# Kernel tuning notes

Hardware: AMD Instinct MI355X
Metric: run time of the kernel (lower is better)

The kernel has to match this reference:

```python
import jax, jax.numpy as jnp
import numpy as np

N_NODES = 100_000
N_EDGES = 800_000
NODE_DIM = 192
CONF_DIM = 64
HID = 256  # graphsage_in == graphsage_hidden
ALPHA = 0.2  # LeakyReLU negative slope


def _lrelu(x):
    return jnp.where(x >= 0, x, ALPHA * x)


def _sage_max(x, src, dst, wl, bl, wr):
    # PyG SAGEConv, aggr='max': out = lin_l(max_{j in N(i)} x_j) + lin_r(x_i)
    msgs = x[src]                                   # [E, HID] gather
    agg = jax.ops.segment_max(msgs, dst, num_segments=N_NODES)  # [N, HID]
    agg = jnp.where(jnp.isneginf(agg), 0.0, agg)    # isolated nodes -> 0
    return agg @ wl + bl + x @ wr


def _mlp2(x, w0, b0, w1, b1):
    # Linear -> LeakyReLU(0.2) -> Linear (activation only between layers)
    return _lrelu(x @ w0 + b0) @ w1 + b1


def setup_inputs() -> dict:
    key = jax.random.key(0)
    ks = jax.random.split(key, 16)
    s = 0.05
    inp = {
        "node_features": jax.random.normal(ks[0], (N_NODES, NODE_DIM), jnp.float32),
        "config_features": jax.random.normal(ks[1], (N_NODES, CONF_DIM), jnp.float32),
        "edges": jax.random.randint(ks[2], (2, N_EDGES), 0, N_NODES, jnp.int32),
        "prenet_w0": jax.random.normal(ks[3], (HID, NODE_DIM), jnp.float32) * s,
        "prenet_b0": jnp.zeros((NODE_DIM,), jnp.float32),
        "prenet_w1": jax.random.normal(ks[4], (NODE_DIM, NODE_DIM), jnp.float32) * s,
        "prenet_b1": jnp.zeros((NODE_DIM,), jnp.float32),
    }
    for l, k0 in ((0, 5), (1, 10)):
        inp[f"sage{l}_wl"] = jax.random.normal(ks[k0], (HID, HID), jnp.float32) * s
        inp[f"sage{l}_bl"] = jnp.zeros((HID,), jnp.float32)
        inp[f"sage{l}_wr"] = jax.random.normal(ks[k0 + 1], (HID, HID), jnp.float32) * s
        inp[f"mlp{l}_w0"] = jax.random.normal(ks[k0 + 2], (HID, NODE_DIM), jnp.float32) * s
        inp[f"mlp{l}_b0"] = jnp.zeros((NODE_DIM,), jnp.float32)
        inp[f"mlp{l}_w1"] = jax.random.normal(ks[k0 + 3], (NODE_DIM, NODE_DIM), jnp.float32) * s
        inp[f"mlp{l}_b1"] = jnp.zeros((NODE_DIM,), jnp.float32)
    return inp


def reference(node_features, config_features, edges,
              prenet_w0, prenet_b0, prenet_w1, prenet_b1,
              sage0_wl, sage0_bl, sage0_wr, mlp0_w0, mlp0_b0, mlp0_w1, mlp0_b1,
              sage1_wl, sage1_bl, sage1_wr, mlp1_w0, mlp1_b0, mlp1_w1, mlp1_b1):
    src, dst = edges[0], edges[1]
    x = jnp.concatenate([config_features, node_features], axis=1)  # [N, 256]
    x = _lrelu(_mlp2(x, prenet_w0, prenet_b0, prenet_w1, prenet_b1))  # [N, 192]
    layers = [
        (sage0_wl, sage0_bl, sage0_wr, mlp0_w0, mlp0_b0, mlp0_w1, mlp0_b1),
        (sage1_wl, sage1_bl, sage1_wr, mlp1_w0, mlp1_b0, mlp1_w1, mlp1_b1),
    ]
    for swl, sbl, swr, mw0, mb0, mw1, mb1 in layers:
        y = jnp.concatenate([config_features, x], axis=1)          # [N, 256]
        y = _sage_max(y, src, dst, swl, sbl, swr)                  # [N, 256]
        y = _lrelu(_mlp2(y, mw0, mb0, mw1, mb1))                   # [N, 192]
        x = x + y
    return x
```

## Files before the change

kernel.cpp:

```cpp
#include <hip/hip_runtime.h>
#include <stdint.h>

#define N_NODES 100000
#define N_EDGES 800000

typedef unsigned short u16;
typedef __attribute__((ext_vector_type(8))) short bf16x8;
typedef __attribute__((ext_vector_type(8))) unsigned short ushort8;
typedef __attribute__((ext_vector_type(4))) float f32x4;
typedef __attribute__((ext_vector_type(4))) int i32x4;
typedef __attribute__((ext_vector_type(4))) unsigned int u32x4;

struct alignas(8) U16x4 { u16 x, y, z, w; };

__device__ __forceinline__ u16 f2b(float f) {
    union { float f; unsigned u; } x; x.f = f;
    unsigned r = (x.u + 0x7FFFu + ((x.u >> 16) & 1u)) >> 16;
    return (u16)r;
}
__device__ __forceinline__ float b2f(u16 h) {
    union { unsigned u; float f; } x; x.u = ((unsigned)h) << 16;
    return x.f;
}
__device__ __forceinline__ u16 keyb(u16 h) {
    u16 m = (u16)((short)h >> 15);
    return (u16)(h ^ (0x8000u | (m & 0x7FFFu)));
}
__device__ __forceinline__ u16 unkey(u16 k) {
    u16 m = (u16)((short)k >> 15);
    return (u16)(k ^ (0x8000u | (~m & 0x7FFFu)));
}
__device__ __forceinline__ unsigned pkmax(unsigned a, unsigned b) {
    unsigned d;
    asm("v_pk_max_u16 %0, %1, %2" : "=v"(d) : "v"(a), "v"(b));
    return d;
}
__device__ __forceinline__ u32x4 pkmax4(u32x4 a, u32x4 b) {
    u32x4 r;
    r.x = pkmax(a.x, b.x); r.y = pkmax(a.y, b.y);
    r.z = pkmax(a.z, b.z); r.w = pkmax(a.w, b.w);
    return r;
}

__device__ __forceinline__ void gload_lds16(const void* g, void* l) {
    __builtin_amdgcn_global_load_lds(
        (const __attribute__((address_space(1))) char*)(uintptr_t)g,
        (__attribute__((address_space(3))) char*)(uintptr_t)l,
        16, 0, 0);
}

__device__ __forceinline__ int simgG(int row, int col) { return row * 136 + col; }
__device__ __forceinline__ int simgF(int row, int col) { return row * 200 + col; }


__global__ void k_prep(const float* __restrict__ conf, const float* __restrict__ node,
                       u16* __restrict__ conf16, u16* __restrict__ node16,
                       u16* __restrict__ keyed, int* __restrict__ deg) {
    const int c4 = N_NODES * 64 / 4;
    const int n4 = N_NODES * 192 / 4;
    int i = blockIdx.x * blockDim.x + threadIdx.x;
    if (i < c4) {
        float4 v = ((const float4*)conf)[i];
        U16x4 o; o.x = f2b(v.x); o.y = f2b(v.y); o.z = f2b(v.z); o.w = f2b(v.w);
        ((U16x4*)conf16)[i] = o;
        U16x4 ko; ko.x = keyb(o.x); ko.y = keyb(o.y); ko.z = keyb(o.z); ko.w = keyb(o.w);
        int n = i >> 4;
        ((U16x4*)keyed)[n * 64 + (i & 15)] = ko;
    } else if (i < c4 + n4) {
        float4 v = ((const float4*)node)[i - c4];
        U16x4 o; o.x = f2b(v.x); o.y = f2b(v.y); o.z = f2b(v.z); o.w = f2b(v.w);
        ((U16x4*)node16)[i - c4] = o;
    } else if (i < c4 + n4 + N_NODES / 4) {
        i32x4 z = {0, 0, 0, 0};
        ((i32x4*)deg)[i - c4 - n4] = z;
    }
}


struct PackSeg { const float* a; const float* b; u16* dst; int K0, K1, Ncol, beg, end; };
struct PackArgs { PackSeg s[8]; };

__global__ void k_pack(PackArgs p, int total) {
    int idx = blockIdx.x * blockDim.x + threadIdx.x;
    if (idx >= total) return;
    #pragma unroll
    for (int si = 0; si < 8; ++si) {
        if (idx >= p.s[si].beg && idx < p.s[si].end) {
            int li = idx - p.s[si].beg;
            int Ncol = p.s[si].Ncol, K0 = p.s[si].K0;
            int kq = li & 7;
            int t = li >> 3;
            int c15 = t & 15; t >>= 4;
            int k8 = t & 3;  t >>= 2;
            int nb = Ncol >> 4;
            int cb = t % nb;
            int ks = t / nb;
            int col = cb * 16 + c15;
            int k = ks * 32 + k8 * 8 + kq;
            float v = (k < K0) ? p.s[si].a[(size_t)k * Ncol + col]
                               : p.s[si].b[(size_t)(k - K0) * Ncol + col];
            p.s[si].dst[li] = f2b(v);
        }
    }
}


__global__ void k_count(const int* __restrict__ dst, int* __restrict__ deg) {
    int e = blockIdx.x * blockDim.x + threadIdx.x;
    if (e < N_EDGES) atomicAdd(&deg[dst[e]], 1);
}

__global__ void k_scan1(const int* __restrict__ deg, int* __restrict__ excl,
                        int* __restrict__ bsum, int n) {
    __shared__ int sh[512];
    int t = threadIdx.x;
    int base = blockIdx.x * 2048 + t * 4;
    int v0 = (base + 0 < n) ? deg[base + 0] : 0;
    int v1 = (base + 1 < n) ? deg[base + 1] : 0;
    int v2 = (base + 2 < n) ? deg[base + 2] : 0;
    int v3 = (base + 3 < n) ? deg[base + 3] : 0;
    int tot = v0 + v1 + v2 + v3;
    sh[t] = tot;
    __syncthreads();
    for (int off = 1; off < 512; off <<= 1) {
        int x = (t >= off) ? sh[t - off] : 0;
        __syncthreads();
        sh[t] += x;
        __syncthreads();
    }
    int run = sh[t] - tot;
    if (base + 0 < n) excl[base + 0] = run; run += v0;
    if (base + 1 < n) excl[base + 1] = run; run += v1;
    if (base + 2 < n) excl[base + 2] = run; run += v2;
    if (base + 3 < n) excl[base + 3] = run;
    if (t == 511) bsum[blockIdx.x] = sh[t];
}

__global__ void k_scan2(int* __restrict__ bsum, int nb) {
    __shared__ int sh[64];
    int t = threadIdx.x;
    int v = (t < nb) ? bsum[t] : 0;
    sh[t] = v;
    __syncthreads();
    for (int off = 1; off < 64; off <<= 1) {
        int x = (t >= off) ? sh[t - off] : 0;
        __syncthreads();
        sh[t] += x;
        __syncthreads();
    }
    if (t < nb) bsum[t] = sh[t] - v;
}

__global__ void k_scan3(int* __restrict__ excl, const int* __restrict__ bsum,
                        int* __restrict__ cursor, int n) {
    int i = blockIdx.x * blockDim.x + threadIdx.x;
    if (i < n) {
        int v = excl[i] + bsum[i >> 11];
        excl[i] = v;
        cursor[i] = v;
    }
}

__global__ void k_scatter(const int* __restrict__ src, const int* __restrict__ dst,
                          int* __restrict__ cursor, int* __restrict__ esrc) {
    int e = blockIdx.x * blockDim.x + threadIdx.x;
    if (e < N_EDGES) {
        int p = atomicAdd(&cursor[dst[e]], 1);
        esrc[p] = src[e];
    }
}


template<int CHUNKS>
__global__ __launch_bounds__(256) void k_agg(
    const u16* __restrict__ keyed,
    const int* __restrict__ indptr, const int* __restrict__ deg,
    const int* __restrict__ iend, const int* __restrict__ esrc,
    u16* __restrict__ agg, u16* __restrict__ aggC) {
    __shared__ int se[512];
    __shared__ int sinfo[2];
    const int b4 = blockIdx.x * 4;
    if (threadIdx.x == 0) {
        sinfo[0] = indptr[b4];
        sinfo[1] = iend[b4 + 3];
    }
    __syncthreads();
    const int sbase = sinfo[0];
    const int slen = sinfo[1] - sbase;
    const bool useLds = slen <= 512;
    if (useLds) {
        for (int i = threadIdx.x; i < slen; i += 256) se[i] = esrc[sbase + i];
    }
    __syncthreads();

    const int node = b4 + (threadIdx.x >> 6);
    const int lane = threadIdx.x & 63;
    constexpr int ACTIVE = (CHUNKS == 32) ? 64 : 48;
    const int e_sub = (CHUNKS == 32) ? (lane >> 5) : (lane >= 24 ? 1 : 0);
    int ch = lane - e_sub * CHUNKS;
    if (ch < 0 || ch >= CHUNKS) ch = 0;
    const int start = indptr[node];
    const int d = deg[node];
    const u16* bp = keyed + ((CHUNKS == 32) ? 0 : 64) + ch * 8;

    u32x4 m = {0u, 0u, 0u, 0u};

    if (lane < ACTIVE && d > 0) {
        const int rounds = (d + 7) >> 3;
        const int lbase = start - sbase;
        for (int rr = 0; rr < rounds; ++rr) {
            const int b0 = rr * 8 + e_sub;
            const int dm1 = d - 1;
            int i0 = min(b0, dm1), i1 = min(b0 + 2, dm1);
            int i2 = min(b0 + 4, dm1), i3 = min(b0 + 6, dm1);
            int s0, s1, s2, s3;
            if (useLds) {
                s0 = se[lbase + i0]; s1 = se[lbase + i1];
                s2 = se[lbase + i2]; s3 = se[lbase + i3];
            } else {
                s0 = esrc[start + i0]; s1 = esrc[start + i1];
                s2 = esrc[start + i2]; s3 = esrc[start + i3];
            }
            u32x4 v0 = *(const u32x4*)(bp + (size_t)s0 * 256);
            u32x4 v1 = *(const u32x4*)(bp + (size_t)s1 * 256);
            u32x4 v2 = *(const u32x4*)(bp + (size_t)s2 * 256);
            u32x4 v3 = *(const u32x4*)(bp + (size_t)s3 * 256);
            m = pkmax4(m, pkmax4(pkmax4(v0, v1), pkmax4(v2, v3)));
        }
    }

    if (CHUNKS == 32) {
        m.x = pkmax(m.x, __shfl_xor(m.x, 32, 64));
        m.y = pkmax(m.y, __shfl_xor(m.y, 32, 64));
        m.z = pkmax(m.z, __shfl_xor(m.z, 32, 64));
        m.w = pkmax(m.w, __shfl_xor(m.w, 32, 64));
    } else {
        m.x = pkmax(m.x, __shfl(m.x, lane + 24, 64));
        m.y = pkmax(m.y, __shfl(m.y, lane + 24, 64));
        m.z = pkmax(m.z, __shfl(m.z, lane + 24, 64));
        m.w = pkmax(m.w, __shfl(m.w, lane + 24, 64));
    }

    unsigned wv[4] = {m.x, m.y, m.z, m.w};
    ushort8 o;
    #pragma unroll
    for (int j = 0; j < 4; ++j) {
        u16 klo = (u16)(wv[j] & 0xFFFFu), khi = (u16)(wv[j] >> 16);
        o[2 * j]     = (d > 0) ? unkey(klo) : (u16)0;
        o[2 * j + 1] = (d > 0) ? unkey(khi) : (u16)0;
    }

    if (CHUNKS == 32) {
        if (lane < 32) {
            *(ushort8*)(agg + (size_t)node * 256 + lane * 8) = o;
            if (lane < 8)
                *(ushort8*)(aggC + (size_t)node * 64 + lane * 8) = o;
        }
    } else {
        if (lane < 24) {
            *(ushort8*)(agg + (size_t)node * 256 + 64 + lane * 8) = o;
        } else if (lane >= 48 && lane < 56) {
            const int c2 = lane - 48;
            ushort8 v = *(const ushort8*)(aggC + (size_t)node * 64 + c2 * 8);
            *(ushort8*)(agg + (size_t)node * 256 + c2 * 8) = v;
        }
    }
}


template<int BN>
__global__ __launch_bounds__(512) void k_gemm(
    const u16* __restrict__ A0, int K0,
    const u16* __restrict__ A1, int K1,
    const u16* __restrict__ A2, int K2,
    const u16* __restrict__ Bt,
    const float* __restrict__ bias,
    u16* __restrict__ outb,
    int nrows)
{
    constexpr int FN = BN / 64;
    constexpr int ASZ = 128 * 32;
    __shared__ u16 lds[2][ASZ + BN * 32] __attribute__((aligned(16)));

    const int tid = threadIdx.x;
    const int wave = tid >> 6;
    const int lane = tid & 63;
    const int wr = wave >> 2;
    const int wc = wave & 3;
    const int rowbase = blockIdx.x * 128;
    const int nk = (K0 + K1 + K2) >> 5;

    const int arow = ((tid >> 6) << 4) | (tid & 15);
    int grow = rowbase + arow; if (grow >= nrows) grow = nrows - 1;
    const int ak8 = (tid >> 4) & 3;
    const u16* segp[3] = {A0, A1, A2};
    const int segK[3] = {K0, K1, K2};
    int seg = 0;
    const u16* gA = segp[0] + (size_t)grow * segK[0] + ak8 * 8;
    int segleft = segK[0] >> 5;
    const u16* gB0 = Bt + (size_t)tid * 8;
    const u16* gB1 = Bt + (size_t)(512 + tid) * 8;
    const int wb = wave * 512;

    auto adv = [&]() {
        gA += 32;
        if (--segleft == 0) {
            while (seg < 2) {
                ++seg;
                if (segK[seg] > 0) {
                    gA = segp[seg] + (size_t)grow * segK[seg] + ak8 * 8;
                    segleft = segK[seg] >> 5;
                    break;
                }
            }
        }
        gB0 += BN * 32;
        gB1 += BN * 32;
    };
    auto stage = [&](int buf) {
        gload_lds16(gA, &lds[buf][wb]);
        gload_lds16(gB0, &lds[buf][ASZ + wb]);
        if constexpr (BN == 256) {
            gload_lds16(gB1, &lds[buf][ASZ + 4096 + wb]);
        } else {
            if (tid < 256) gload_lds16(gB1, &lds[buf][ASZ + 4096 + wb]);
        }
    };

    f32x4 zero = {0.f, 0.f, 0.f, 0.f};
    f32x4 acc[4][FN];
    #pragma unroll
    for (int fm = 0; fm < 4; ++fm)
        #pragma unroll
        for (int fn = 0; fn < FN; ++fn)
            acc[fm][fn] = zero;

    stage(0); adv();
    __syncthreads();

    const int l15 = lane & 15, l4 = lane >> 4;

    for (int ks = 0; ks < nk; ++ks) {
        const int cur = ks & 1;
        if (ks + 1 < nk) { stage(cur ^ 1); adv(); }
        const u16* la = &lds[cur][0];
        const u16* lb = &lds[cur][ASZ];
        bf16x8 a[4], b[FN];
        #pragma unroll
        for (int fm = 0; fm < 4; ++fm)
            a[fm] = *(const bf16x8*)(la + (wr * 4 + fm) * 512 + lane * 8);
        #pragma unroll
        for (int fn = 0; fn < FN; ++fn)
            b[fn] = *(const bf16x8*)(lb + (wc * FN + fn) * 512 + lane * 8);
        #pragma unroll
        for (int fm = 0; fm < 4; ++fm)
            #pragma unroll
            for (int fn = 0; fn < FN; ++fn)
                acc[fm][fn] = __builtin_amdgcn_mfma_f32_16x16x32_bf16(a[fm], b[fn], acc[fm][fn], 0, 0, 0);
        __syncthreads();
    }

    u16* sbuf = &lds[0][0];
    #pragma unroll
    for (int chunk = 0; chunk < 2; ++chunk) {
        if ((wc >> 1) == chunk) {
            const int cbase = (wc & 1) * 64;
            #pragma unroll
            for (int fn = 0; fn < FN; ++fn) {
                const int cp = cbase + fn * 16 + l15;
                const float bs = bias[chunk * 128 + cp];
                #pragma unroll
                for (int fm = 0; fm < 4; ++fm) {
                    const int rbase = wr * 64 + fm * 16 + l4 * 4;
                    #pragma unroll
                    for (int r = 0; r < 4; ++r)
                        sbuf[simgG(rbase + r, cp)] = f2b(acc[fm][fn][r] + bs);
                }
            }
        }
        __syncthreads();
        #pragma unroll
        for (int j = 0; j < 4; ++j) {
            const int chk = j * 512 + tid;
            const int row = chk >> 4;
            const int cp = (chk & 15) * 8;
            const int gr = rowbase + row;
            if (gr < nrows) {
                ushort8 hv = *(const ushort8*)&sbuf[simgG(row, cp)];
                *(ushort8*)(outb + (size_t)gr * 256 + chunk * 128 + cp) = hv;
            }
        }
        __syncthreads();
    }
}


template<int EPI>
__global__ __launch_bounds__(512) void k_fused(
    const u16* __restrict__ A0, int K0,
    const u16* __restrict__ A1, int K1,
    const u16* __restrict__ B1t, const float* __restrict__ bias1,
    const u16* __restrict__ B2t, const float* __restrict__ bias2,
    float* __restrict__ outf, u16* __restrict__ outb,
    const u16* __restrict__ resid16, u16* __restrict__ keyed,
    int nrows)
{
    __shared__ u16 lds[25592] __attribute__((aligned(16)));

    const int tid = threadIdx.x;
    const int wave = tid >> 6;
    const int lane = tid & 63;
    const int wr = wave >> 2;
    const int wc = wave & 3;
    const int l15 = lane & 15, l4 = lane >> 4;
    const int rowbase = blockIdx.x * 128;
    const int nk1 = (K0 + K1) >> 5;

    const int arow = ((tid >> 6) << 4) | (tid & 15);
    int grow = rowbase + arow; if (grow >= nrows) grow = nrows - 1;
    const int ak8 = (tid >> 4) & 3;
    const u16* gA = A0 + (size_t)grow * K0 + ak8 * 8;
    int segleft = K0 >> 5;
    const u16* gB0 = B1t + (size_t)tid * 8;
    const u16* gB1 = B1t + (size_t)(512 + tid) * 8;
    const int wb = wave * 512;

    auto adv = [&]() {
        gA += 32;
        if (--segleft == 0 && K1 > 0) {
            gA = A1 + (size_t)grow * K1 + ak8 * 8;
            segleft = K1 >> 5;
        }
        gB0 += 6144;
        gB1 += 6144;
    };
    auto stage = [&](int buf) {
        gload_lds16(gA, &lds[buf * 4096 + wb]);
        gload_lds16(gB0, &lds[8192 + buf * 6144 + wb]);
        if (tid < 256) gload_lds16(gB1, &lds[8192 + buf * 6144 + 4096 + wb]);
    };

    f32x4 zero = {0.f, 0.f, 0.f, 0.f};
    f32x4 acc[4][3];
    #pragma unroll
    for (int fm = 0; fm < 4; ++fm)
        #pragma unroll
        for (int fn = 0; fn < 3; ++fn)
            acc[fm][fn] = zero;

    stage(0); adv();
    __syncthreads();

    for (int ks = 0; ks < nk1; ++ks) {
        const int cur = ks & 1;
        if (ks + 1 < nk1) { stage(cur ^ 1); adv(); }
        const u16* la = &lds[cur * 4096];
        const u16* lb = &lds[8192 + cur * 6144];
        bf16x8 a[4], b[3];
        #pragma unroll
        for (int fm = 0; fm < 4; ++fm)
            a[fm] = *(const bf16x8*)(la + (wr * 4 + fm) * 512 + lane * 8);
        #pragma unroll
        for (int fn = 0; fn < 3; ++fn)
            b[fn] = *(const bf16x8*)(lb + (wc * 3 + fn) * 512 + lane * 8);
        #pragma unroll
        for (int fm = 0; fm < 4; ++fm)
            #pragma unroll
            for (int fn = 0; fn < 3; ++fn)
                acc[fm][fn] = __builtin_amdgcn_mfma_f32_16x16x32_bf16(a[fm], b[fn], acc[fm][fn], 0, 0, 0);
        __syncthreads();
    }

    {
        const int c0 = wc * 48;
        #pragma unroll
        for (int fn = 0; fn < 3; ++fn) {
            const int c = c0 + fn * 16 + l15;
            const float bs = bias1[c];
            const int coff = (c >> 5) * 4096 + ((c >> 3) & 3) * 128 + (c & 7);
            #pragma unroll
            for (int fm = 0; fm < 4; ++fm) {
                const int rb = wr * 4 + fm;
                #pragma unroll
                for (int rr = 0; rr < 4; ++rr) {
                    const int r16 = l4 * 4 + rr;
                    float v = acc[fm][fn][rr] + bs;
                    v = (v >= 0.f) ? v : 0.2f * v;
                    lds[coff + rb * 512 + r16 * 8] = f2b(v);
                }
            }
        }
    }
    __syncthreads();

    bf16x8 breg[18];
    #pragma unroll
    for (int ks = 0; ks < 6; ++ks)
        #pragma unroll
        for (int fn = 0; fn < 3; ++fn)
            breg[ks * 3 + fn] = *(const bf16x8*)(B2t + (size_t)(ks * 12 + wc * 3 + fn) * 512 + lane * 8);

    f32x4 acc2[4][3];
    #pragma unroll
    for (int fm = 0; fm < 4; ++fm)
        #pragma unroll
        for (int fn = 0; fn < 3; ++fn)
            acc2[fm][fn] = zero;

    #pragma unroll
    for (int ks = 0; ks < 6; ++ks) {
        bf16x8 a2[4];
        #pragma unroll
        for (int fm = 0; fm < 4; ++fm)
            a2[fm] = *(const bf16x8*)(&lds[ks * 4096 + (wr * 4 + fm) * 512 + lane * 8]);
        #pragma unroll
        for (int fm = 0; fm < 4; ++fm)
            #pragma unroll
            for (int fn = 0; fn < 3; ++fn)
                acc2[fm][fn] = __builtin_amdgcn_mfma_f32_16x16x32_bf16(a2[fm], breg[ks * 3 + fn], acc2[fm][fn], 0, 0, 0);
    }
    __syncthreads();

    {
        const int c0 = wc * 48;
        #pragma unroll
        for (int fn = 0; fn < 3; ++fn) {
            const int c = c0 + fn * 16 + l15;
            const float bs = bias2[c];
            #pragma unroll
            for (int fm = 0; fm < 4; ++fm) {
                const int rbase = wr * 64 + fm * 16 + l4 * 4;
                #pragma unroll
                for (int r = 0; r < 4; ++r) {
                    float v = acc2[fm][fn][r] + bs;
                    v = (v >= 0.f) ? v : 0.2f * v;
                    lds[simgF(rbase + r, c)] = f2b(v);
                }
            }
        }
    }
    __syncthreads();

    #pragma unroll
    for (int j = 0; j < 6; ++j) {
        const int chk = j * 512 + tid;
        const int row = chk / 24;
        const int c = (chk - row * 24) * 8;
        const int gr = rowbase + row;
        if (gr < nrows) {
            ushort8 hv = *(const ushort8*)&lds[simgF(row, c)];
            if (EPI == 4) {
                ushort8 rv = *(const ushort8*)(resid16 + (size_t)gr * 192 + c);
                f32x4 o0, o1;
                #pragma unroll
                for (int k = 0; k < 4; ++k) {
                    o0[k] = b2f(hv[k]) + b2f(rv[k]);
                    o1[k] = b2f(hv[k + 4]) + b2f(rv[k + 4]);
                }
                *(f32x4*)(outf + (size_t)gr * 192 + c) = o0;
                *(f32x4*)(outf + (size_t)gr * 192 + c + 4) = o1;
            } else if (EPI == 5) {
                *(ushort8*)(outb + (size_t)gr * 192 + c) = hv;
                ushort8 kv;
                #pragma unroll
                for (int k = 0; k < 8; ++k) kv[k] = keyb(hv[k]);
                *(ushort8*)(keyed + (size_t)gr * 256 + 64 + c) = kv;
            } else {
                ushort8 rv = *(const ushort8*)(resid16 + (size_t)gr * 192 + c);
                ushort8 nb, kv;
                #pragma unroll
                for (int k = 0; k < 8; ++k) {
                    u16 hb = f2b(b2f(hv[k]) + b2f(rv[k]));
                    nb[k] = hb;
                    kv[k] = keyb(hb);
                }
                *(ushort8*)(outb + (size_t)gr * 192 + c) = nb;
                *(ushort8*)(keyed + (size_t)gr * 256 + 64 + c) = kv;
            }
        }
    }
}


extern "C" void kernel_launch(void* const* d_in, const int* in_sizes, int n_in,
                              void* d_out, int out_size, void* d_ws, size_t ws_size,
                              hipStream_t stream)
{
    (void)in_sizes; (void)n_in; (void)out_size; (void)ws_size;
    const float* node = (const float*)d_in[0];
    const float* conf = (const float*)d_in[1];
    const int* edges  = (const int*)d_in[2];
    const float* pw0  = (const float*)d_in[3];
    const float* pb0  = (const float*)d_in[4];
    const float* pw1  = (const float*)d_in[5];
    const float* pb1  = (const float*)d_in[6];
    const float* W[14];
    for (int i = 0; i < 14; ++i) W[i] = (const float*)d_in[7 + i];
    float* out = (float*)d_out;
    const int* e_src = edges;
    const int* e_dst = edges + N_EDGES;

    u16* keyed = (u16*)d_out;

    char* w = (char*)d_ws;
    auto alloc = [&](size_t b) { char* p = w; w += (b + 255) & ~(size_t)255; return p; };
    u16* conf16 = (u16*)alloc((size_t)N_NODES * 64 * 2);
    u16* node16 = (u16*)alloc((size_t)N_NODES * 192 * 2);
    u16* x16    = (u16*)alloc((size_t)N_NODES * 192 * 2);
    u16* agg16  = (u16*)alloc((size_t)N_NODES * 256 * 2);
    u16* aggC   = (u16*)alloc((size_t)N_NODES * 64 * 2);
    int* deg    = (int*)alloc((size_t)N_NODES * 4);
    int* indptr = (int*)alloc((size_t)N_NODES * 4);
    int* cursor = (int*)alloc((size_t)N_NODES * 4);
    int* esrc   = (int*)alloc((size_t)N_EDGES * 4);
    int* bsum   = (int*)alloc(4096);
    u16* pw0t   = (u16*)alloc((size_t)192 * 256 * 2);
    u16* pw1t   = (u16*)alloc((size_t)192 * 192 * 2);
    u16 *sB[2], *mw0t[2], *mw1t[2];
    for (int l = 0; l < 2; ++l) {
        sB[l]   = (u16*)alloc((size_t)256 * 512 * 2);
        mw0t[l] = (u16*)alloc((size_t)192 * 256 * 2);
        mw1t[l] = (u16*)alloc((size_t)192 * 192 * 2);
    }

    {
        const int tot = N_NODES * 64 / 4 + N_NODES * 192 / 4 + N_NODES / 4;
        k_prep<<<(tot + 255) / 256, 256, 0, stream>>>(conf, node, conf16, node16, keyed, deg);
    }
    {
        PackArgs pa;
        int off = 0;
        auto seg = [&](int i, const float* a, int K0, const float* b, int K1, int Ncol, u16* dst) {
            int sz = Ncol * (K0 + K1);
            pa.s[i] = {a, b, dst, K0, K1, Ncol, off, off + sz};
            off += sz;
        };
        seg(0, pw0, 256, nullptr, 0, 192, pw0t);
        seg(1, pw1, 192, nullptr, 0, 192, pw1t);
        seg(2, W[0], 256, W[2], 256, 256, sB[0]);
        seg(3, W[3], 256, nullptr, 0, 192, mw0t[0]);
        seg(4, W[5], 192, nullptr, 0, 192, mw1t[0]);
        seg(5, W[7], 256, W[9], 256, 256, sB[1]);
        seg(6, W[10], 256, nullptr, 0, 192, mw0t[1]);
        seg(7, W[12], 192, nullptr, 0, 192, mw1t[1]);
        k_pack<<<(off + 255) / 256, 256, 0, stream>>>(pa, off);
    }
    k_count<<<(N_EDGES + 255) / 256, 256, 0, stream>>>(e_dst, deg);
    int nb = (N_NODES + 2047) / 2048;
    k_scan1<<<nb, 512, 0, stream>>>(deg, indptr, bsum, N_NODES);
    k_scan2<<<1, 64, 0, stream>>>(bsum, nb);
    k_scan3<<<(N_NODES + 255) / 256, 256, 0, stream>>>(indptr, bsum, cursor, N_NODES);
    k_scatter<<<(N_EDGES + 255) / 256, 256, 0, stream>>>(e_src, e_dst, cursor, esrc);

    const int gblk = (N_NODES + 127) / 128;
    k_fused<5><<<gblk, 512, 0, stream>>>(conf16, 64, node16, 192,
                                         pw0t, pb0, pw1t, pb1,
                                         nullptr, x16, nullptr, keyed, N_NODES);
    for (int l = 0; l < 2; ++l) {
        if (l == 0)
            k_agg<32><<<N_NODES / 4, 256, 0, stream>>>(keyed, indptr, deg, cursor, esrc, agg16, aggC);
        else
            k_agg<24><<<N_NODES / 4, 256, 0, stream>>>(keyed, indptr, deg, cursor, esrc, agg16, aggC);
        k_gemm<256><<<gblk, 512, 0, stream>>>(agg16, 256, conf16, 64, x16, 192,
                                              sB[l], W[7*l+1], agg16, N_NODES);
        if (l == 0)
            k_fused<6><<<gblk, 512, 0, stream>>>(agg16, 256, nullptr, 0,
                                                 mw0t[0], W[4], mw1t[0], W[6],
                                                 nullptr, x16, x16, keyed, N_NODES);
        else
            k_fused<4><<<gblk, 512, 0, stream>>>(agg16, 256, nullptr, 0,
                                                 mw0t[1], W[11], mw1t[1], W[13],
                                                 out, nullptr, x16, nullptr, N_NODES);
    }
}
```

Before: 444.1 us.

## Fuse SAGE linear GEMM with following MLP into one per-layer kernel

Replaces the separate SAGE GEMM kernel and MLP kernel with a single k_layer kernel per layer. The SAGE output tile stays in LDS as bf16 and feeds the two MLP GEMMs directly, so the [N,256] intermediate is never written to or re-read from global memory. B weights are now loaded straight from global memory into registers with double buffering, not staged through LDS. This removes one launch and one round trip through global memory per layer, but it puts more pressure on registers and LDS (a single 80KB LDS buffer), which may reduce occupancy.

```diff
diff --git a/kernel.cpp b/kernel.cpp
--- a/kernel.cpp
+++ b/kernel.cpp
@@ -49,8 +49,10 @@
         16, 0, 0);
 }
 
-__device__ __forceinline__ int simgG(int row, int col) { return row * 136 + col; }
 __device__ __forceinline__ int simgF(int row, int col) { return row * 200 + col; }
+__device__ __forceinline__ int fimg(int row, int c) {
+    return (c >> 5) * 4096 + ((c >> 3) & 3) * 128 + (c & 7) + (row >> 4) * 512 + (row & 15) * 8;
+}
 
 
 __global__ void k_prep(const float* __restrict__ conf, const float* __restrict__ node,
@@ -268,133 +270,6 @@
 }
 
 
-template<int BN>
-__global__ __launch_bounds__(512) void k_gemm(
-    const u16* __restrict__ A0, int K0,
-    const u16* __restrict__ A1, int K1,
-    const u16* __restrict__ A2, int K2,
-    const u16* __restrict__ Bt,
-    const float* __restrict__ bias,
-    u16* __restrict__ outb,
-    int nrows)
-{
-    constexpr int FN = BN / 64;
-    constexpr int ASZ = 128 * 32;
-    __shared__ u16 lds[2][ASZ + BN * 32] __attribute__((aligned(16)));
-
-    const int tid = threadIdx.x;
-    const int wave = tid >> 6;
-    const int lane = tid & 63;
-    const int wr = wave >> 2;
-    const int wc = wave & 3;
-    const int rowbase = blockIdx.x * 128;
-    const int nk = (K0 + K1 + K2) >> 5;
-
-    const int arow = ((tid >> 6) << 4) | (tid & 15);
-    int grow = rowbase + arow; if (grow >= nrows) grow = nrows - 1;
-    const int ak8 = (tid >> 4) & 3;
-    const u16* segp[3] = {A0, A1, A2};
-    const int segK[3] = {K0, K1, K2};
-    int seg = 0;
-    const u16* gA = segp[0] + (size_t)grow * segK[0] + ak8 * 8;
-    int segleft = segK[0] >> 5;
-    const u16* gB0 = Bt + (size_t)tid * 8;
-    const u16* gB1 = Bt + (size_t)(512 + tid) * 8;
-    const int wb = wave * 512;
-
-    auto adv = [&]() {
-        gA += 32;
-        if (--segleft == 0) {
-            while (seg < 2) {
-                ++seg;
-                if (segK[seg] > 0) {
-                    gA = segp[seg] + (size_t)grow * segK[seg] + ak8 * 8;
-                    segleft = segK[seg] >> 5;
-                    break;
-                }
-            }
-        }
-        gB0 += BN * 32;
-        gB1 += BN * 32;
-    };
-    auto stage = [&](int buf) {
-        gload_lds16(gA, &lds[buf][wb]);
-        gload_lds16(gB0, &lds[buf][ASZ + wb]);
-        if constexpr (BN == 256) {
-            gload_lds16(gB1, &lds[buf][ASZ + 4096 + wb]);
-        } else {
-            if (tid < 256) gload_lds16(gB1, &lds[buf][ASZ + 4096 + wb]);
-        }
-    };
-
-    f32x4 zero = {0.f, 0.f, 0.f, 0.f};
-    f32x4 acc[4][FN];
-    #pragma unroll
-    for (int fm = 0; fm < 4; ++fm)
-        #pragma unroll
-        for (int fn = 0; fn < FN; ++fn)
-            acc[fm][fn] = zero;
-
-    stage(0); adv();
-    __syncthreads();
-
-    const int l15 = lane & 15, l4 = lane >> 4;
-
-    for (int ks = 0; ks < nk; ++ks) {
-        const int cur = ks & 1;
-        if (ks + 1 < nk) { stage(cur ^ 1); adv(); }
-        const u16* la = &lds[cur][0];
-        const u16* lb = &lds[cur][ASZ];
-        bf16x8 a[4], b[FN];
-        #pragma unroll
-        for (int fm = 0; fm < 4; ++fm)
-            a[fm] = *(const bf16x8*)(la + (wr * 4 + fm) * 512 + lane * 8);
-        #pragma unroll
-        for (int fn = 0; fn < FN; ++fn)
-            b[fn] = *(const bf16x8*)(lb + (wc * FN + fn) * 512 + lane * 8);
-        #pragma unroll
-        for (int fm = 0; fm < 4; ++fm)
-            #pragma unroll
-            for (int fn = 0; fn < FN; ++fn)
-                acc[fm][fn] = __builtin_amdgcn_mfma_f32_16x16x32_bf16(a[fm], b[fn], acc[fm][fn], 0, 0, 0);
-        __syncthreads();
-    }
-
-    u16* sbuf = &lds[0][0];
-    #pragma unroll
-    for (int chunk = 0; chunk < 2; ++chunk) {
-        if ((wc >> 1) == chunk) {
-            const int cbase = (wc & 1) * 64;
-            #pragma unroll
-            for (int fn = 0; fn < FN; ++fn) {
-                const int cp = cbase + fn * 16 + l15;
-                const float bs = bias[chunk * 128 + cp];
-                #pragma unroll
-                for (int fm = 0; fm < 4; ++fm) {
-                    const int rbase = wr * 64 + fm * 16 + l4 * 4;
-                    #pragma unroll
-                    for (int r = 0; r < 4; ++r)
-                        sbuf[simgG(rbase + r, cp)] = f2b(acc[fm][fn][r] + bs);
-                }
-            }
-        }
-        __syncthreads();
-        #pragma unroll
-        for (int j = 0; j < 4; ++j) {
-            const int chk = j * 512 + tid;
-            const int row = chk >> 4;
-            const int cp = (chk & 15) * 8;
-            const int gr = rowbase + row;
-            if (gr < nrows) {
-                ushort8 hv = *(const ushort8*)&sbuf[simgG(row, cp)];
-                *(ushort8*)(outb + (size_t)gr * 256 + chunk * 128 + cp) = hv;
-            }
-        }
-        __syncthreads();
-    }
-}
-
-
 template<int EPI>
 __global__ __launch_bounds__(512) void k_fused(
     const u16* __restrict__ A0, int K0,
@@ -477,16 +352,14 @@
         for (int fn = 0; fn < 3; ++fn) {
             const int c = c0 + fn * 16 + l15;
             const float bs = bias1[c];
-            const int coff = (c >> 5) * 4096 + ((c >> 3) & 3) * 128 + (c & 7);
             #pragma unroll
             for (int fm = 0; fm < 4; ++fm) {
                 const int rb = wr * 4 + fm;
                 #pragma unroll
                 for (int rr = 0; rr < 4; ++rr) {
-                    const int r16 = l4 * 4 + rr;
                     float v = acc[fm][fn][rr] + bs;
                     v = (v >= 0.f) ? v : 0.2f * v;
-                    lds[coff + rb * 512 + r16 * 8] = f2b(v);
+                    lds[fimg(rb * 16 + l4 * 4 + rr, c)] = f2b(v);
                 }
             }
         }
@@ -549,8 +422,222 @@
         const int gr = rowbase + row;
         if (gr < nrows) {
             ushort8 hv = *(const ushort8*)&lds[simgF(row, c)];
+            *(ushort8*)(outb + (size_t)gr * 192 + c) = hv;
+            ushort8 kv;
+            #pragma unroll
+            for (int k = 0; k < 8; ++k) kv[k] = keyb(hv[k]);
+            *(ushort8*)(keyed + (size_t)gr * 256 + 64 + c) = kv;
+        }
+    }
+    (void)outf; (void)resid16;
+}
+
+
+template<int EPI>
+__global__ __launch_bounds__(512) void k_layer(
+    const u16* __restrict__ A0, const u16* __restrict__ A1, const u16* __restrict__ A2,
+    const u16* __restrict__ sBt, const float* __restrict__ bl,
+    const u16* __restrict__ B1t, const float* __restrict__ bias1,
+    const u16* __restrict__ B2t, const float* __restrict__ bias2,
+    float* __restrict__ outf, u16* __restrict__ outb,
+    const u16* __restrict__ resid16, u16* __restrict__ keyed,
+    int nrows)
+{
+    __shared__ u16 lds[40960] __attribute__((aligned(16)));
+
+    const int tid = threadIdx.x;
+    const int wave = tid >> 6;
+    const int lane = tid & 63;
+    const int wr = wave >> 2;
+    const int wc = wave & 3;
+    const int l15 = lane & 15, l4 = lane >> 4;
+    const int rowbase = blockIdx.x * 128;
+
+    const int arow = (wave << 4) | (tid & 15);
+    int grow = rowbase + arow; if (grow >= nrows) grow = nrows - 1;
+    const int ak8 = (tid >> 4) & 3;
+    const u16* segp[3] = {A0, A1, A2};
+    const int segK[3] = {256, 64, 192};
+    int seg = 0;
+    const u16* gA = segp[0] + (size_t)grow * 256 + ak8 * 8;
+    int segleft = 256 >> 5;
+    const int wb = wave * 512;
+    auto advA = [&]() {
+        gA += 32;
+        if (--segleft == 0 && seg < 2) {
+            ++seg;
+            gA = segp[seg] + (size_t)grow * segK[seg] + ak8 * 8;
+            segleft = segK[seg] >> 5;
+        }
+    };
+
+    f32x4 zero = {0.f, 0.f, 0.f, 0.f};
+    f32x4 acc[4][4];
+    #pragma unroll
+    for (int fm = 0; fm < 4; ++fm)
+        #pragma unroll
+        for (int fn = 0; fn < 4; ++fn)
+            acc[fm][fn] = zero;
+
+    gload_lds16(gA, &lds[wb]); advA();
+    bf16x8 bb[2][4];
+    #pragma unroll
+    for (int fn = 0; fn < 4; ++fn)
+        bb[0][fn] = *(const bf16x8*)(sBt + (size_t)(wc * 4 + fn) * 512 + lane * 8);
+    __syncthreads();
+
+    #pragma unroll
+    for (int ks = 0; ks < 16; ++ks) {
+        const int cur = ks & 1;
+        if (ks + 1 < 16) {
+            gload_lds16(gA, &lds[(cur ^ 1) * 4096 + wb]); advA();
+            #pragma unroll
+            for (int fn = 0; fn < 4; ++fn)
+                bb[cur ^ 1][fn] = *(const bf16x8*)(sBt + (size_t)((ks + 1) * 16 + wc * 4 + fn) * 512 + lane * 8);
+        }
+        bf16x8 a[4];
+        #pragma unroll
+        for (int fm = 0; fm < 4; ++fm)
+            a[fm] = *(const bf16x8*)(&lds[cur * 4096 + (wr * 4 + fm) * 512 + lane * 8]);
+        #pragma unroll
+        for (int fm = 0; fm < 4; ++fm)
+            #pragma unroll
+            for (int fn = 0; fn < 4; ++fn)
+                acc[fm][fn] = __builtin_amdgcn_mfma_f32_16x16x32_bf16(a[fm], bb[cur][fn], acc[fm][fn], 0, 0, 0);
+        __syncthreads();
+    }
+
+    {
+        const int c0 = wc * 64;
+        #pragma unroll
+        for (int fn = 0; fn < 4; ++fn) {
+            const int c = c0 + fn * 16 + l15;
+            const float bs = bl[c];
+            #pragma unroll
+            for (int fm = 0; fm < 4; ++fm) {
+                const int rb = wr * 4 + fm;
+                #pragma unroll
+                for (int rr = 0; rr < 4; ++rr)
+                    lds[8192 + fimg(rb * 16 + l4 * 4 + rr, c)] = f2b(acc[fm][fn][rr] + bs);
+            }
+        }
+    }
+    __syncthreads();
+
+    f32x4 acc2[4][3];
+    #pragma unroll
+    for (int fm = 0; fm < 4; ++fm)
+        #pragma unroll
+        for (int fn = 0; fn < 3; ++fn)
+            acc2[fm][fn] = zero;
+
+    bf16x8 b2[2][3];
+    #pragma unroll
+    for (int fn = 0; fn < 3; ++fn)
+        b2[0][fn] = *(const bf16x8*)(B1t + (size_t)(wc * 3 + fn) * 512 + lane * 8);
+
+    #pragma unroll
+    for (int ks = 0; ks < 8; ++ks) {
+        const int cur = ks & 1;
+        if (ks + 1 < 8) {
+            #pragma unroll
+            for (int fn = 0; fn < 3; ++fn)
+                b2[cur ^ 1][fn] = *(const bf16x8*)(B1t + (size_t)((ks + 1) * 12 + wc * 3 + fn) * 512 + lane * 8);
+        }
+        bf16x8 a2[4];
+        #pragma unroll
+        for (int fm = 0; fm < 4; ++fm)
+            a2[fm] = *(const bf16x8*)(&lds[8192 + ks * 4096 + (wr * 4 + fm) * 512 + lane * 8]);
+        #pragma unroll
+        for (int fm = 0; fm < 4; ++fm)
+            #pragma unroll
+            for (int fn = 0; fn < 3; ++fn)
+                acc2[fm][fn] = __builtin_amdgcn_mfma_f32_16x16x32_bf16(a2[fm], b2[cur][fn], acc2[fm][fn], 0, 0, 0);
+    }
+    __syncthreads();
+
+    {
+        const int c0 = wc * 48;
+        #pragma unroll
+        for (int fn = 0; fn < 3; ++fn) {
+            const int c = c0 + fn * 16 + l15;
+            const float bs = bias1[c];
+            #pragma unroll
+            for (int fm = 0; fm < 4; ++fm) {
+                const int rb = wr * 4 + fm;
+                #pragma unroll
+                for (int rr = 0; rr < 4; ++rr) {
+                    float v = acc2[fm][fn][rr] + bs;
+                    v = (v >= 0.f) ? v : 0.2f * v;
+                    lds[8192 + fimg(rb * 16 + l4 * 4 + rr, c)] = f2b(v);
+                }
+            }
+        }
+    }
+    __syncthreads();
+
+    f32x4 acc3[4][3];
+    #pragma unroll
+    for (int fm = 0; fm < 4; ++fm)
+        #pragma unroll
+        for (int fn = 0; fn < 3; ++fn)
+            acc3[fm][fn] = zero;
+
+    bf16x8 b3[2][3];
+    #pragma unroll
+    for (int fn = 0; fn < 3; ++fn)
+        b3[0][fn] = *(const bf16x8*)(B2t + (size_t)(wc * 3 + fn) * 512 + lane * 8);
+
+    #pragma unroll
+    for (int ks = 0; ks < 6; ++ks) {
+        const int cur = ks & 1;
+        if (ks + 1 < 6) {
+            #pragma unroll
+            for (int fn = 0; fn < 3; ++fn)
+                b3[cur ^ 1][fn] = *(const bf16x8*)(B2t + (size_t)((ks + 1) * 12 + wc * 3 + fn) * 512 + lane * 8);
+        }
+        bf16x8 a3[4];
+        #pragma unroll
+        for (int fm = 0; fm < 4; ++fm)
+            a3[fm] = *(const bf16x8*)(&lds[8192 + ks * 4096 + (wr * 4 + fm) * 512 + lane * 8]);
+        #pragma unroll
+        for (int fm = 0; fm < 4; ++fm)
+            #pragma unroll
+            for (int fn = 0; fn < 3; ++fn)
+                acc3[fm][fn] = __builtin_amdgcn_mfma_f32_16x16x32_bf16(a3[fm], b3[cur][fn], acc3[fm][fn], 0, 0, 0);
+    }
+    __syncthreads();
+
+    {
+        const int c0 = wc * 48;
+        #pragma unroll
+        for (int fn = 0; fn < 3; ++fn) {
+            const int c = c0 + fn * 16 + l15;
+            const float bs = bias2[c];
+            #pragma unroll
+            for (int fm = 0; fm < 4; ++fm) {
+                const int rbase = wr * 64 + fm * 16 + l4 * 4;
+                #pragma unroll
+                for (int r = 0; r < 4; ++r) {
+                    float v = acc3[fm][fn][r] + bs;
+                    v = (v >= 0.f) ? v : 0.2f * v;
+                    lds[8192 + simgF(rbase + r, c)] = f2b(v);
+                }
+            }
+        }
+    }
+    __syncthreads();
+
+    #pragma unroll
+    for (int j = 0; j < 6; ++j) {
+        const int chk = j * 512 + tid;
+        const int row = chk / 24;
+        const int c = (chk - row * 24) * 8;
+        const int gr = rowbase + row;
+        if (gr < nrows) {
+            ushort8 hv = *(const ushort8*)&lds[8192 + simgF(row, c)];
+            ushort8 rv = *(const ushort8*)(resid16 + (size_t)gr * 192 + c);
             if (EPI == 4) {
-                ushort8 rv = *(const ushort8*)(resid16 + (size_t)gr * 192 + c);
                 f32x4 o0, o1;
                 #pragma unroll
                 for (int k = 0; k < 4; ++k) {
@@ -559,14 +646,7 @@
                 }
                 *(f32x4*)(outf + (size_t)gr * 192 + c) = o0;
                 *(f32x4*)(outf + (size_t)gr * 192 + c + 4) = o1;
-            } else if (EPI == 5) {
-                *(ushort8*)(outb + (size_t)gr * 192 + c) = hv;
-                ushort8 kv;
-                #pragma unroll
-                for (int k = 0; k < 8; ++k) kv[k] = keyb(hv[k]);
-                *(ushort8*)(keyed + (size_t)gr * 256 + 64 + c) = kv;
             } else {
-                ushort8 rv = *(const ushort8*)(resid16 + (size_t)gr * 192 + c);
                 ushort8 nb, kv;
                 #pragma unroll
                 for (int k = 0; k < 8; ++k) {
@@ -656,20 +736,12 @@
     k_fused<5><<<gblk, 512, 0, stream>>>(conf16, 64, node16, 192,
                                          pw0t, pb0, pw1t, pb1,
                                          nullptr, x16, nullptr, keyed, N_NODES);
-    for (int l = 0; l < 2; ++l) {
-        if (l == 0)
-            k_agg<32><<<N_NODES / 4, 256, 0, stream>>>(keyed, indptr, deg, cursor, esrc, agg16, aggC);
-        else
-            k_agg<24><<<N_NODES / 4, 256, 0, stream>>>(keyed, indptr, deg, cursor, esrc, agg16, aggC);
-        k_gemm<256><<<gblk, 512, 0, stream>>>(agg16, 256, conf16, 64, x16, 192,
-                                              sB[l], W[7*l+1], agg16, N_NODES);
-        if (l == 0)
-            k_fused<6><<<gblk, 512, 0, stream>>>(agg16, 256, nullptr, 0,
-                                                 mw0t[0], W[4], mw1t[0], W[6],
-                                                 nullptr, x16, x16, keyed, N_NODES);
-        else
-            k_fused<4><<<gblk, 512, 0, stream>>>(agg16, 256, nullptr, 0,
-                                                 mw0t[1], W[11], mw1t[1], W[13],
-                                                 out, nullptr, x16, nullptr, N_NODES);
-    }
-}
+    k_agg<32><<<N_NODES / 4, 256, 0, stream>>>(keyed, indptr, deg, cursor, esrc, agg16, aggC);
+    k_layer<6><<<gblk, 512, 0, stream>>>(agg16, conf16, x16,
+                                         sB[0], W[1], mw0t[0], W[4], mw1t[0], W[6],
+                                         nullptr, x16, x16, keyed, N_NODES);
+    k_agg<24><<<N_NODES / 4, 256, 0, stream>>>(keyed, indptr, deg, cursor, esrc, agg16, aggC);
+    k_layer<4><<<gblk, 512, 0, stream>>>(agg16, conf16, x16,
+                                         sB[1], W[8], mw0t[1], W[11], mw1t[1], W[13],
+                                         out, nullptr, x16, nullptr, N_NODES);
+}
```

New measurement: 469.7 us. 5.8% more time.
